# Optimization experiments

Measured on AMD Instinct MI355X. Metric: run time of the kernel, lower is better.

Reference implementation:

```python
import jax, jax.numpy as jnp
import numpy as np

B, L = 64, 512
D_IN, D_POS = 256, 64
KS, VS, H = 64, 64, 8
OUT = 256
EPS = 1e-5
NEG = -1e30


def setup_inputs() -> dict:
    key = jax.random.key(0)
    ks = jax.random.split(key, 12)
    D = D_IN + D_POS
    s = 0.02
    return {
        "emb": jax.random.normal(ks[0], (B, L, D_IN), jnp.float32),
        "boxes": jax.random.normal(ks[1], (B, L, D_POS), jnp.float32),
        "lengths": jax.random.randint(ks[2], (B,), 1, L + 1, jnp.int32),
        "Wq": jax.random.normal(ks[3], (D, H * KS), jnp.float32) * s,
        "Wk": jax.random.normal(ks[4], (D, H * KS), jnp.float32) * s,
        "Wv": jax.random.normal(ks[5], (D, H * VS), jnp.float32) * s,
        "W1": jax.random.normal(ks[6], (H * VS, OUT), jnp.float32) * s,
        "b1": jnp.zeros((OUT,), jnp.float32),
        "W2": jax.random.normal(ks[7], (OUT, OUT), jnp.float32) * s,
        "b2": jnp.zeros((OUT,), jnp.float32),
        "g1": jnp.ones((OUT,), jnp.float32),
        "be1": jnp.zeros((OUT,), jnp.float32),
        "g2": jnp.ones((OUT,), jnp.float32),
        "be2": jnp.zeros((OUT,), jnp.float32),
    }


def masked_bn(x, m, cnt, gamma, beta):
    # BatchNorm1d (training stats) over valid tokens only; x: [B,L,C], m: [B,L,1]
    mean = jnp.sum(x * m, axis=(0, 1)) / cnt
    var = jnp.sum(((x - mean) ** 2) * m, axis=(0, 1)) / cnt
    return gamma * (x - mean) * jax.lax.rsqrt(var + EPS) + beta


def reference(emb, boxes, lengths, Wq, Wk, Wv, W1, b1, W2, b2, g1, be1, g2, be2):
    X = jnp.concatenate([emb, boxes], axis=-1)  # [B,L,D]
    valid = (jnp.arange(L)[None, :] < lengths[:, None])  # [B,L] bool
    m = valid[..., None].astype(X.dtype)  # [B,L,1]
    cnt = jnp.sum(m)

    D = X.shape[-1]
    Q = jnp.einsum('bld,dhk->bhlk', X, Wq.reshape(D, H, KS))
    K = jnp.einsum('bld,dhk->bhlk', X, Wk.reshape(D, H, KS))
    V = jnp.einsum('bld,dhv->bhlv', X, Wv.reshape(D, H, VS))

    scores = jnp.einsum('bhqk,bhmk->bhqm', Q, K) / jnp.sqrt(jnp.float32(KS))
    scores = jnp.where(valid[:, None, None, :], scores, NEG)  # mask keys
    A = jax.nn.softmax(scores, axis=-1)  # [B,H,L,L]
    Z = jnp.einsum('bhqm,bhmv->bhqv', A, V)  # [B,H,L,V]
    Z = jnp.transpose(Z, (0, 2, 1, 3)).reshape(B, L, H * VS)

    # agregate: Linear -> BN -> ReLU -> (dropout=identity, eval) -> Linear -> BN + skip -> ReLU
    Z1 = Z @ W1 + b1
    Z1 = jax.nn.relu(masked_bn(Z1, m, cnt, g1, be1)) * m
    Z2 = Z1 @ W2 + b2
    out = jax.nn.relu(masked_bn(Z2, m, cnt, g2, be2) + emb) * m
    return out  # padded [B,L,OUT]; invalid positions zeroed
```

## Files before the change

kernel.cpp:

```cpp
#include <hip/hip_runtime.h>
#include <hip/hip_bf16.h>
#include <cstdio>

#define B_    64
#define L_    512
#define DIN   256
#define DPOS  64
#define DD    320
#define HH    8
#define ROWS  (B_*L_)
#define NQKV  1536

typedef __attribute__((ext_vector_type(4))) float floatx4;
typedef __attribute__((ext_vector_type(8))) __bf16 bf16x8;
typedef __attribute__((ext_vector_type(4))) __bf16 bf16x4;

static __device__ __forceinline__ floatx4 mfma_bf16(bf16x8 a, bf16x8 b, floatx4 c) {
  return __builtin_amdgcn_mfma_f32_16x16x32_bf16(a, b, c, 0, 0, 0);
}

#define GLOAD_LDS(gp, lp) \
  __builtin_amdgcn_global_load_lds((const __attribute__((address_space(1))) void*)(gp), \
                                   (__attribute__((address_space(3))) void*)(lp), 16, 0, 0)

__global__ __launch_bounds__(256)
void prep_emb(const float* __restrict__ emb, __hip_bfloat16* __restrict__ X) {
  int idx = blockIdx.x * 256 + threadIdx.x;
  int row = idx >> 6, c4 = (idx & 63) * 4;
  const float4 v = *(const float4*)(emb + (size_t)idx * 4);
  bf16x4 o; o[0] = (__bf16)v.x; o[1] = (__bf16)v.y; o[2] = (__bf16)v.z; o[3] = (__bf16)v.w;
  *(bf16x4*)((__bf16*)X + (size_t)row * DD + c4) = o;
}

__global__ __launch_bounds__(256)
void prep_box(const float* __restrict__ boxes, __hip_bfloat16* __restrict__ X) {
  int idx = blockIdx.x * 256 + threadIdx.x;
  int row = idx >> 4, c4 = (idx & 15) * 4;
  const float4 v = *(const float4*)(boxes + (size_t)idx * 4);
  bf16x4 o; o[0] = (__bf16)v.x; o[1] = (__bf16)v.y; o[2] = (__bf16)v.z; o[3] = (__bf16)v.w;
  *(bf16x4*)((__bf16*)X + (size_t)row * DD + DIN + c4) = o;
}

__global__ __launch_bounds__(256)
void prep_w(const float* __restrict__ Wq, const float* __restrict__ Wk,
            const float* __restrict__ Wv, const float* __restrict__ W1,
            const float* __restrict__ W2,
            __hip_bfloat16* __restrict__ WqkvT, __hip_bfloat16* __restrict__ W1T,
            __hip_bfloat16* __restrict__ W2T) {
  __shared__ float tile[64][65];
  int blk = blockIdx.x, t = threadIdx.x;
  const float* src; __hip_bfloat16* dst; int n0, k0, ldsrc, lddst;
  if (blk < 120) {
    int m = blk / 40, rel = blk % 40;
    src = (m == 0) ? Wq : (m == 1) ? Wk : Wv;
    dst = WqkvT + (size_t)m * 512 * DD;
    n0 = (rel / 5) * 64; k0 = (rel % 5) * 64; ldsrc = 512; lddst = DD;
  } else if (blk < 152) {
    int rel = blk - 120;
    src = W1; dst = W1T; n0 = (rel >> 3) * 64; k0 = (rel & 7) * 64; ldsrc = 256; lddst = 512;
  } else {
    int rel = blk - 152;
    src = W2; dst = W2T; n0 = (rel >> 2) * 64; k0 = (rel & 3) * 64; ldsrc = 256; lddst = 256;
  }
#pragma unroll
  for (int i = 0; i < 16; ++i) {
    int e = i * 256 + t, kr = e >> 6, nc = e & 63;
    tile[kr][nc] = src[(size_t)(k0 + kr) * ldsrc + n0 + nc];
  }
  __syncthreads();
#pragma unroll
  for (int i = 0; i < 4; ++i) {
    int ww = i * 256 + t, nr = ww >> 4, kc = (ww & 15) * 4;
    bf16x4 o;
    o[0] = (__bf16)tile[kc][nr];   o[1] = (__bf16)tile[kc+1][nr];
    o[2] = (__bf16)tile[kc+2][nr]; o[3] = (__bf16)tile[kc+3][nr];
    *(bf16x4*)(dst + (size_t)(n0 + nr) * lddst + k0 + kc) = o;
  }
}

template<int EPI>
__global__ __launch_bounds__(256)
void gemm_bt(const __hip_bfloat16* __restrict__ A, const __hip_bfloat16* __restrict__ BT,
             int nbx, int N, int K, int lda,
             float* __restrict__ outF, const float* __restrict__ bias,
             __hip_bfloat16* __restrict__ outQK, __hip_bfloat16* __restrict__ outVT,
             const int* __restrict__ lengths, float* __restrict__ pS,
             float* __restrict__ pS2) {
  __shared__ __align__(16) __bf16 sm[32768];
  int hw = blockIdx.x;
  int lidx = (hw & 7) * ((int)gridDim.x >> 3) + (hw >> 3);
  int bx = lidx % nbx, by = lidx / nbx;
  int t = threadIdx.x;
  int m0 = by * 128, n0 = bx * 128;
  int lenb = lengths[m0 >> 9];
  if ((m0 & 511) >= lenb) {
    if (EPI == 1 && t < 128) {
      pS [by*256 + bx*128 + t] = 0.f;
      pS2[by*256 + bx*128 + t] = 0.f;
    }
    return;
  }
  int wave = t >> 6, lane = t & 63, lr = lane & 15, lg = lane >> 4;
  int wr = wave >> 1, wc = wave & 1;
  floatx4 acc[4][4];
#pragma unroll
  for (int i = 0; i < 4; ++i)
#pragma unroll
    for (int j = 0; j < 4; ++j)
#pragma unroll
      for (int q = 0; q < 4; ++q) acc[i][j][q] = 0.f;

  int srow = t >> 3;
  int scb = (t & 7) ^ (srow & 7);
  const __bf16* gA = (const __bf16*)A + (size_t)(m0 + srow) * lda + scb * 8;
  const __bf16* gB = (const __bf16*)BT + (size_t)(n0 + srow) * K + scb * 8;

  auto stage = [&](int k0, int buf) {
    __bf16* Ad = sm + buf * 8192;
    __bf16* Bd = sm + 16384 + buf * 8192;
#pragma unroll
    for (int r = 0; r < 4; ++r) {
      GLOAD_LDS(gA + (size_t)(r*32) * lda + k0, Ad + (r*256 + t) * 8);
      GLOAD_LDS(gB + (size_t)(r*32) * K   + k0, Bd + (r*256 + t) * 8);
    }
  };

  int aoff[4][2], boff[4][2];
#pragma unroll
  for (int i = 0; i < 4; ++i) {
#pragma unroll
    for (int ks = 0; ks < 2; ++ks) {
      int ra = wr*64 + i*16 + lr;
      int rb = wc*64 + i*16 + lr;
      aoff[i][ks] = ra*64 + (((ks*4 + lg) ^ (ra & 7)) * 8);
      boff[i][ks] = rb*64 + (((ks*4 + lg) ^ (rb & 7)) * 8);
    }
  }

  int NK = K >> 6;
  stage(0, 0);
  __syncthreads();
  for (int kt = 0; kt < NK; ++kt) {
    int cur = kt & 1;
    if (kt + 1 < NK) stage((kt + 1) << 6, cur ^ 1);
    const __bf16* As = sm + cur * 8192;
    const __bf16* Bs = sm + 16384 + cur * 8192;
#pragma unroll
    for (int ks = 0; ks < 2; ++ks) {
      bf16x8 af[4], bfr[4];
#pragma unroll
      for (int i = 0; i < 4; ++i) af[i]  = *(const bf16x8*)(As + aoff[i][ks]);
#pragma unroll
      for (int j = 0; j < 4; ++j) bfr[j] = *(const bf16x8*)(Bs + boff[j][ks]);
      __builtin_amdgcn_s_setprio(1);
#pragma unroll
      for (int i = 0; i < 4; ++i)
#pragma unroll
        for (int j = 0; j < 4; ++j)
          acc[i][j] = mfma_bf16(af[i], bfr[j], acc[i][j]);
      __builtin_amdgcn_s_setprio(0);
    }
    __syncthreads();
  }

  if (EPI == 1) {
    int lbase = m0 & 511;
    float s1[4] = {0.f,0.f,0.f,0.f}, s2[4] = {0.f,0.f,0.f,0.f};
#pragma unroll
    for (int i = 0; i < 4; ++i)
#pragma unroll
      for (int j = 0; j < 4; ++j)
#pragma unroll
        for (int q = 0; q < 4; ++q) {
          int rrow = wr*64 + i*16 + lg*4 + q;
          int col = n0 + wc*64 + j*16 + lr;
          float v = acc[i][j][q] + bias[col];
          outF[(size_t)(m0 + rrow) * N + col] = v;
          if (lbase + rrow < lenb) { s1[j] += v; s2[j] += v*v; }
        }
#pragma unroll
    for (int j = 0; j < 4; ++j) {
      s1[j] += __shfl_xor(s1[j], 16); s1[j] += __shfl_xor(s1[j], 32);
      s2[j] += __shfl_xor(s2[j], 16); s2[j] += __shfl_xor(s2[j], 32);
    }
    float* fb = (float*)sm;
    if (lg == 0) {
#pragma unroll
      for (int j = 0; j < 4; ++j) {
        int cloc = wc*64 + j*16 + lr;
        fb[wr*128 + cloc] = s1[j];
        fb[256 + wr*128 + cloc] = s2[j];
      }
    }
    __syncthreads();
    if (t < 128) {
      pS [by*256 + bx*128 + t] = fb[t] + fb[128 + t];
      pS2[by*256 + bx*128 + t] = fb[256 + t] + fb[384 + t];
    }
  } else if (n0 < 1024) {
#pragma unroll
    for (int i = 0; i < 4; ++i)
#pragma unroll
      for (int j = 0; j < 4; ++j)
#pragma unroll
        for (int q = 0; q < 4; ++q) {
          int row = m0 + wr*64 + i*16 + lg*4 + q;
          int col = n0 + wc*64 + j*16 + lr;
          outQK[(size_t)row * 1024 + col] = __float2bfloat16(acc[i][j][q]);
        }
  } else {
    __bf16* Ct = sm;
#pragma unroll
    for (int i = 0; i < 4; ++i)
#pragma unroll
      for (int j = 0; j < 4; ++j) {
        int col = wc*64 + j*16 + lr;
        int row0 = wr*64 + i*16 + lg*4;
        bf16x4 pv;
#pragma unroll
        for (int q = 0; q < 4; ++q) pv[q] = (__bf16)acc[i][j][q];
        *(bf16x4*)(Ct + col*136 + row0) = pv;
      }
    __syncthreads();
    int b = m0 >> 9, l0 = m0 & 511, gcol0 = n0 - 1024;
#pragma unroll
    for (int it = 0; it < 8; ++it) {
      int g = it * 256 + t;
      int vv = g >> 4, rc = g & 15;
      bf16x8 val = *(const bf16x8*)(Ct + vv*136 + rc*8);
      int gc = gcol0 + vv, h = gc >> 6, vg = gc & 63;
      *(bf16x8*)((__bf16*)outVT + ((size_t)((b*HH + h)*64 + vg))*512 + l0 + rc*8) = val;
    }
  }
}

__global__ __launch_bounds__(512)
void attn(__hip_bfloat16* QK, const __hip_bfloat16* __restrict__ VT,
          const int* __restrict__ lengths) {
  int hw = blockIdx.x;
  int h = hw & 7, qt = (hw >> 3) & 3, b = hw >> 5;
  int len = lengths[b];
  if (qt * 128 >= len) return;
  __shared__ __align__(16) __hip_bfloat16 Ks[2][4096];
  __shared__ __align__(16) __hip_bfloat16 Vs[2][4096];
  __shared__ __align__(16) __hip_bfloat16 P[8][16][72];
  int t = threadIdx.x, wave = t >> 6, lane = t & 63, lr = lane & 15, lg = lane >> 4;
  int q0 = qt * 128 + wave * 16;
  const __hip_bfloat16* Qb = QK + (size_t)b*512*1024 + h*64;
  const __hip_bfloat16* Kb = QK + (size_t)b*512*1024 + 512 + h*64;
  const __hip_bfloat16* Vb = VT + (size_t)(b*HH + h)*64*512;

  bf16x8 qf0 = *(const bf16x8*)(Qb + (size_t)(q0 + lr)*1024 + lg*8);
  bf16x8 qf1 = *(const bf16x8*)(Qb + (size_t)(q0 + lr)*1024 + 32 + lg*8);
#pragma unroll
  for (int i = 0; i < 8; ++i) {
    qf0[i] = (__bf16)((float)qf0[i] * 0.125f);
    qf1[i] = (__bf16)((float)qf1[i] * 0.125f);
  }
  bf16x8 onesf;
#pragma unroll
  for (int i = 0; i < 8; ++i) onesf[i] = (__bf16)1.0f;

  int off0[4], off1[4];
#pragma unroll
  for (int r4 = 0; r4 < 4; ++r4) {
    int row = r4*16 + lr, sw = row & 7;
    off0[r4] = row*64 + ((lg ^ sw) * 8);
    off1[r4] = row*64 + (((lg + 4) ^ sw) * 8);
  }
  int srow = t >> 3, scb = t & 7;
  int scbd = scb ^ (srow & 7);
  const __hip_bfloat16* kgp = Kb + (size_t)srow*1024 + scbd*8;
  const __hip_bfloat16* vgp = Vb + (size_t)srow*512 + scbd*8;

  int nt = (len + 63) >> 6;

  auto stage = [&](int kt, int buf) {
    GLOAD_LDS(kgp + (size_t)kt*65536, &Ks[buf][t*8]);
    GLOAD_LDS(vgp + kt*64, &Vs[buf][t*8]);
  };

  floatx4 O[4];
  floatx4 Ol = {0.f, 0.f, 0.f, 0.f};
#pragma unroll
  for (int vb = 0; vb < 4; ++vb)
#pragma unroll
    for (int i = 0; i < 4; ++i) O[vb][i] = 0.f;

  stage(0, 0);
  __syncthreads();

  for (int kt = 0; kt < nt; ++kt) {
    int cur = kt & 1;
    if (kt + 1 < nt) stage(kt + 1, cur ^ 1);
    int kb0 = kt * 64;
    const __hip_bfloat16* Kc = Ks[cur];
    const __hip_bfloat16* Vc = Vs[cur];

    floatx4 S[4];
    __builtin_amdgcn_s_setprio(1);
#pragma unroll
    for (int kb = 0; kb < 4; ++kb) {
      bf16x8 kf0 = *(const bf16x8*)(Kc + off0[kb]);
      bf16x8 kf1 = *(const bf16x8*)(Kc + off1[kb]);
      floatx4 s = {0.f, 0.f, 0.f, 0.f};
      s = mfma_bf16(kf0, qf0, s);
      s = mfma_bf16(kf1, qf1, s);
      S[kb] = s;
    }
    __builtin_amdgcn_s_setprio(0);
#pragma unroll
    for (int kb = 0; kb < 4; ++kb)
#pragma unroll
      for (int i = 0; i < 4; ++i) S[kb][i] = __expf(S[kb][i]);
    if (kb0 + 64 > len) {
#pragma unroll
      for (int kb = 0; kb < 4; ++kb)
#pragma unroll
        for (int i = 0; i < 4; ++i)
          if (kb0 + kb*16 + lg*4 + i >= len) S[kb][i] = 0.f;
    }
#pragma unroll
    for (int kb = 0; kb < 4; ++kb) {
      bf16x4 pv;
#pragma unroll
      for (int i = 0; i < 4; ++i) pv[i] = (__bf16)S[kb][i];
      *(bf16x4*)(&P[wave][lr][kb*16 + lg*4]) = pv;
    }
    bf16x8 pf0 = *(const bf16x8*)(&P[wave][lr][lg*8]);
    bf16x8 pf1 = *(const bf16x8*)(&P[wave][lr][32 + lg*8]);
    __builtin_amdgcn_s_setprio(1);
#pragma unroll
    for (int vb = 0; vb < 4; ++vb) {
      bf16x8 vf0 = *(const bf16x8*)(Vc + off0[vb]);
      bf16x8 vf1 = *(const bf16x8*)(Vc + off1[vb]);
      O[vb] = mfma_bf16(pf0, vf0, O[vb]);
      O[vb] = mfma_bf16(pf1, vf1, O[vb]);
    }
    Ol = mfma_bf16(pf0, onesf, Ol);
    Ol = mfma_bf16(pf1, onesf, Ol);
    __builtin_amdgcn_s_setprio(0);
    __syncthreads();
  }

#pragma unroll
  for (int vb = 0; vb < 4; ++vb)
#pragma unroll
    for (int i = 0; i < 4; ++i) {
      int q = q0 + lg*4 + i;
      float z = O[vb][i] / Ol[i];
      QK[(size_t)(b*512 + q)*1024 + h*64 + vb*16 + lr] = __float2bfloat16(z);
    }
}

__global__ __launch_bounds__(256)
void stats_fin(const float* __restrict__ pS, const float* __restrict__ pS2,
               const int* __restrict__ lengths, const float* __restrict__ g,
               const float* __restrict__ be, float* __restrict__ aff) {
  int t = threadIdx.x;
  float cnt = 0.f;
  for (int i = 0; i < 64; ++i) cnt += (float)lengths[i];
  float s = 0.f, s2 = 0.f;
  for (int i = 0; i < 256; ++i) { s += pS[i*256 + t]; s2 += pS2[i*256 + t]; }
  float mean = s / cnt;
  float var = s2 / cnt - mean * mean;
  float a = g[t] * rsqrtf(var + 1e-5f);
  aff[t] = a;
  aff[256 + t] = be[t] - mean * a;
}

__global__ __launch_bounds__(256)
void apply1(const float* __restrict__ Zr, const int* __restrict__ lengths,
            const float* __restrict__ aff, __hip_bfloat16* __restrict__ Zn) {
  int idx = blockIdx.x * 256 + threadIdx.x;
  int row = idx >> 6, c4 = (idx & 63) * 4;
  int b = row >> 9, l = row & 511;
  bool ok = l < lengths[b];
  float4 v = *(const float4*)(Zr + (size_t)row*256 + c4);
  float4 a = *(const float4*)(aff + c4);
  float4 c = *(const float4*)(aff + 256 + c4);
  bf16x4 o;
  o[0] = (__bf16)(ok ? fmaxf(a.x*v.x + c.x, 0.f) : 0.f);
  o[1] = (__bf16)(ok ? fmaxf(a.y*v.y + c.y, 0.f) : 0.f);
  o[2] = (__bf16)(ok ? fmaxf(a.z*v.z + c.z, 0.f) : 0.f);
  o[3] = (__bf16)(ok ? fmaxf(a.w*v.w + c.w, 0.f) : 0.f);
  *(bf16x4*)((__bf16*)Zn + (size_t)row*256 + c4) = o;
}

__global__ __launch_bounds__(256)
void apply2(const float* __restrict__ Zr, const float* __restrict__ emb,
            const int* __restrict__ lengths, const float* __restrict__ aff,
            float* __restrict__ out) {
  int idx = blockIdx.x * 256 + threadIdx.x;
  int row = idx >> 6, c4 = (idx & 63) * 4;
  int b = row >> 9, l = row & 511;
  bool ok = l < lengths[b];
  size_t base = (size_t)row*256 + c4;
  float4 v = *(const float4*)(Zr + base);
  float4 e = *(const float4*)(emb + base);
  float4 a = *(const float4*)(aff + c4);
  float4 c = *(const float4*)(aff + 256 + c4);
  float4 o;
  o.x = ok ? fmaxf(a.x*v.x + c.x + e.x, 0.f) : 0.f;
  o.y = ok ? fmaxf(a.y*v.y + c.y + e.y, 0.f) : 0.f;
  o.z = ok ? fmaxf(a.z*v.z + c.z + e.z, 0.f) : 0.f;
  o.w = ok ? fmaxf(a.w*v.w + c.w + e.w, 0.f) : 0.f;
  *(float4*)(out + base) = o;
}

extern "C" void kernel_launch(void* const* d_in, const int* in_sizes, int n_in,
                              void* d_out, int out_size, void* d_ws, size_t ws_size,
                              hipStream_t stream) {
  const float* emb   = (const float*)d_in[0];
  const float* boxes = (const float*)d_in[1];
  const int*   dlen  = (const int*)d_in[2];
  const float* Wq    = (const float*)d_in[3];
  const float* Wk    = (const float*)d_in[4];
  const float* Wv    = (const float*)d_in[5];
  const float* W1    = (const float*)d_in[6];
  const float* b1    = (const float*)d_in[7];
  const float* W2    = (const float*)d_in[8];
  const float* b2    = (const float*)d_in[9];
  const float* g1    = (const float*)d_in[10];
  const float* be1   = (const float*)d_in[11];
  const float* g2    = (const float*)d_in[12];
  const float* be2   = (const float*)d_in[13];
  float* out = (float*)d_out;

  const size_t oWqkvT = 0;
  const size_t oW1T   = 983040;
  const size_t oW2T   = 1245184;
  const size_t oAff1  = 1376256;
  const size_t oAff2  = 1378304;
  const size_t oPS    = 1380352;
  const size_t oPS2   = 1642496;
  const size_t oXbf   = 1904640;
  const size_t oQK    = 22876160;
  const size_t oVT    = 89985024;
  const size_t NEED   = 123539456;
  if (ws_size < NEED) { fprintf(stderr, "ws too small: %zu < %zu\n", ws_size, NEED); return; }

  char* w = (char*)d_ws;
  __hip_bfloat16* WqkvT = (__hip_bfloat16*)(w + oWqkvT);
  __hip_bfloat16* W1T   = (__hip_bfloat16*)(w + oW1T);
  __hip_bfloat16* W2T   = (__hip_bfloat16*)(w + oW2T);
  float* aff1 = (float*)(w + oAff1);
  float* aff2 = (float*)(w + oAff2);
  float* pS   = (float*)(w + oPS);
  float* pS2  = (float*)(w + oPS2);
  __hip_bfloat16* Xbf = (__hip_bfloat16*)(w + oXbf);
  __hip_bfloat16* Z1n = (__hip_bfloat16*)(w + oXbf);
  __hip_bfloat16* QK  = (__hip_bfloat16*)(w + oQK);
  float* Z2raw = (float*)(w + oQK);
  __hip_bfloat16* VT  = (__hip_bfloat16*)(w + oVT);
  float* Z1raw = (float*)(w + oVT);

  prep_emb<<<ROWS/4, 256, 0, stream>>>(emb, Xbf);
  prep_box<<<ROWS/16, 256, 0, stream>>>(boxes, Xbf);
  prep_w<<<168, 256, 0, stream>>>(Wq, Wk, Wv, W1, W2, WqkvT, W1T, W2T);
  gemm_bt<0><<<12*256, 256, 0, stream>>>(
      Xbf, WqkvT, 12, NQKV, DD, DD, nullptr, nullptr, QK, VT,
      dlen, nullptr, nullptr);
  attn<<<2048, 512, 0, stream>>>(QK, VT, dlen);
  gemm_bt<1><<<2*256, 256, 0, stream>>>(
      QK, W1T, 2, 256, 512, 1024, Z1raw, b1, nullptr, nullptr,
      dlen, pS, pS2);
  stats_fin<<<1, 256, 0, stream>>>(pS, pS2, dlen, g1, be1, aff1);
  apply1<<<ROWS/4, 256, 0, stream>>>(Z1raw, dlen, aff1, Z1n);
  gemm_bt<1><<<2*256, 256, 0, stream>>>(
      Z1n, W2T, 2, 256, 256, 256, Z2raw, b2, nullptr, nullptr,
      dlen, pS, pS2);
  stats_fin<<<1, 256, 0, stream>>>(pS, pS2, dlen, g2, be2, aff2);
  apply2<<<ROWS/4, 256, 0, stream>>>(Z2raw, emb, dlen, aff2, out);
}
```

Measured before the change: 158.1 us.

## Shrink attention key tiles, use exp2, parallelize stats and skip padded rows

The attention key/value tile shrinks from 64 to 32 keys per step. This lowers LDS use and tightens length tail waste, and K and V staging is split across the two halves of the block. The softmax switches to exp2, with log2(e) folded into the query scale. stats_fin now reduces with 1024 threads instead of a serial 256-row loop. The two prep kernels merge into one launch, and apply1 and apply2 skip reading padded rows beyond each sequence length. Smaller tiles double the loop iterations and barriers per key block.

Result: slower. 167.5 us (+6.0%).

```diff
diff --git a/kernel.cpp b/kernel.cpp
--- a/kernel.cpp
+++ b/kernel.cpp
@@ -24,21 +24,22 @@
                                    (__attribute__((address_space(3))) void*)(lp), 16, 0, 0)
 
 __global__ __launch_bounds__(256)
-void prep_emb(const float* __restrict__ emb, __hip_bfloat16* __restrict__ X) {
-  int idx = blockIdx.x * 256 + threadIdx.x;
-  int row = idx >> 6, c4 = (idx & 63) * 4;
-  const float4 v = *(const float4*)(emb + (size_t)idx * 4);
-  bf16x4 o; o[0] = (__bf16)v.x; o[1] = (__bf16)v.y; o[2] = (__bf16)v.z; o[3] = (__bf16)v.w;
-  *(bf16x4*)((__bf16*)X + (size_t)row * DD + c4) = o;
-}
-
-__global__ __launch_bounds__(256)
-void prep_box(const float* __restrict__ boxes, __hip_bfloat16* __restrict__ X) {
-  int idx = blockIdx.x * 256 + threadIdx.x;
-  int row = idx >> 4, c4 = (idx & 15) * 4;
-  const float4 v = *(const float4*)(boxes + (size_t)idx * 4);
-  bf16x4 o; o[0] = (__bf16)v.x; o[1] = (__bf16)v.y; o[2] = (__bf16)v.z; o[3] = (__bf16)v.w;
-  *(bf16x4*)((__bf16*)X + (size_t)row * DD + DIN + c4) = o;
+void prep_x(const float* __restrict__ emb, const float* __restrict__ boxes,
+            __hip_bfloat16* __restrict__ X) {
+  int bb = blockIdx.x;
+  if (bb < ROWS/4) {
+    int idx = bb * 256 + threadIdx.x;
+    int row = idx >> 6, c4 = (idx & 63) * 4;
+    const float4 v = *(const float4*)(emb + (size_t)idx * 4);
+    bf16x4 o; o[0] = (__bf16)v.x; o[1] = (__bf16)v.y; o[2] = (__bf16)v.z; o[3] = (__bf16)v.w;
+    *(bf16x4*)((__bf16*)X + (size_t)row * DD + c4) = o;
+  } else {
+    int idx = (bb - ROWS/4) * 256 + threadIdx.x;
+    int row = idx >> 4, c4 = (idx & 15) * 4;
+    const float4 v = *(const float4*)(boxes + (size_t)idx * 4);
+    bf16x4 o; o[0] = (__bf16)v.x; o[1] = (__bf16)v.y; o[2] = (__bf16)v.z; o[3] = (__bf16)v.w;
+    *(bf16x4*)((__bf16*)X + (size_t)row * DD + DIN + c4) = o;
+  }
 }
 
 __global__ __launch_bounds__(256)
@@ -241,9 +242,9 @@
   int h = hw & 7, qt = (hw >> 3) & 3, b = hw >> 5;
   int len = lengths[b];
   if (qt * 128 >= len) return;
-  __shared__ __align__(16) __hip_bfloat16 Ks[2][4096];
-  __shared__ __align__(16) __hip_bfloat16 Vs[2][4096];
-  __shared__ __align__(16) __hip_bfloat16 P[8][16][72];
+  __shared__ __align__(16) __hip_bfloat16 Ks[2][2048];
+  __shared__ __align__(16) __hip_bfloat16 Vs[2][2048];
+  __shared__ __align__(16) __hip_bfloat16 P[8][16][40];
   int t = threadIdx.x, wave = t >> 6, lane = t & 63, lr = lane & 15, lg = lane >> 4;
   int q0 = qt * 128 + wave * 16;
   const __hip_bfloat16* Qb = QK + (size_t)b*512*1024 + h*64;
@@ -254,30 +255,37 @@
   bf16x8 qf1 = *(const bf16x8*)(Qb + (size_t)(q0 + lr)*1024 + 32 + lg*8);
 #pragma unroll
   for (int i = 0; i < 8; ++i) {
-    qf0[i] = (__bf16)((float)qf0[i] * 0.125f);
-    qf1[i] = (__bf16)((float)qf1[i] * 0.125f);
+    qf0[i] = (__bf16)((float)qf0[i] * 0.18033688f);
+    qf1[i] = (__bf16)((float)qf1[i] * 0.18033688f);
   }
   bf16x8 onesf;
 #pragma unroll
   for (int i = 0; i < 8; ++i) onesf[i] = (__bf16)1.0f;
 
-  int off0[4], off1[4];
-#pragma unroll
-  for (int r4 = 0; r4 < 4; ++r4) {
-    int row = r4*16 + lr, sw = row & 7;
-    off0[r4] = row*64 + ((lg ^ sw) * 8);
-    off1[r4] = row*64 + (((lg + 4) ^ sw) * 8);
-  }
-  int srow = t >> 3, scb = t & 7;
-  int scbd = scb ^ (srow & 7);
-  const __hip_bfloat16* kgp = Kb + (size_t)srow*1024 + scbd*8;
-  const __hip_bfloat16* vgp = Vb + (size_t)srow*512 + scbd*8;
-
-  int nt = (len + 63) >> 6;
+  int koff0[2], koff1[2];
+#pragma unroll
+  for (int kb = 0; kb < 2; ++kb) {
+    int row = kb*16 + lr, sw = row & 7;
+    koff0[kb] = row*64 + ((lg ^ sw) * 8);
+    koff1[kb] = row*64 + (((lg + 4) ^ sw) * 8);
+  }
+  int voff[4];
+#pragma unroll
+  for (int vb = 0; vb < 4; ++vb) {
+    int row = vb*16 + lr;
+    voff[vb] = row*32 + ((lg ^ (row & 3)) * 8);
+  }
+  int ku = t & 255;
+  int krow = ku >> 3, kcb = (ku & 7) ^ (krow & 7);
+  const __hip_bfloat16* kgp = Kb + (size_t)krow*1024 + kcb*8;
+  int vrow = ku >> 2, vcb = (ku & 3) ^ (vrow & 3);
+  const __hip_bfloat16* vgp = Vb + (size_t)vrow*512 + vcb*8;
+
+  int nt = (len + 31) >> 5;
 
   auto stage = [&](int kt, int buf) {
-    GLOAD_LDS(kgp + (size_t)kt*65536, &Ks[buf][t*8]);
-    GLOAD_LDS(vgp + kt*64, &Vs[buf][t*8]);
+    if (t < 256) GLOAD_LDS(kgp + (size_t)kt*32768, &Ks[buf][ku*8]);
+    else         GLOAD_LDS(vgp + kt*32,           &Vs[buf][ku*8]);
   };
 
   floatx4 O[4];
@@ -293,16 +301,16 @@
   for (int kt = 0; kt < nt; ++kt) {
     int cur = kt & 1;
     if (kt + 1 < nt) stage(kt + 1, cur ^ 1);
-    int kb0 = kt * 64;
+    int kb0 = kt * 32;
     const __hip_bfloat16* Kc = Ks[cur];
     const __hip_bfloat16* Vc = Vs[cur];
 
-    floatx4 S[4];
+    floatx4 S[2];
     __builtin_amdgcn_s_setprio(1);
 #pragma unroll
-    for (int kb = 0; kb < 4; ++kb) {
-      bf16x8 kf0 = *(const bf16x8*)(Kc + off0[kb]);
-      bf16x8 kf1 = *(const bf16x8*)(Kc + off1[kb]);
+    for (int kb = 0; kb < 2; ++kb) {
+      bf16x8 kf0 = *(const bf16x8*)(Kc + koff0[kb]);
+      bf16x8 kf1 = *(const bf16x8*)(Kc + koff1[kb]);
       floatx4 s = {0.f, 0.f, 0.f, 0.f};
       s = mfma_bf16(kf0, qf0, s);
       s = mfma_bf16(kf1, qf1, s);
@@ -310,35 +318,31 @@
     }
     __builtin_amdgcn_s_setprio(0);
 #pragma unroll
-    for (int kb = 0; kb < 4; ++kb)
-#pragma unroll
-      for (int i = 0; i < 4; ++i) S[kb][i] = __expf(S[kb][i]);
-    if (kb0 + 64 > len) {
-#pragma unroll
-      for (int kb = 0; kb < 4; ++kb)
+    for (int kb = 0; kb < 2; ++kb)
+#pragma unroll
+      for (int i = 0; i < 4; ++i) S[kb][i] = __builtin_amdgcn_exp2f(S[kb][i]);
+    if (kb0 + 32 > len) {
+#pragma unroll
+      for (int kb = 0; kb < 2; ++kb)
 #pragma unroll
         for (int i = 0; i < 4; ++i)
           if (kb0 + kb*16 + lg*4 + i >= len) S[kb][i] = 0.f;
     }
 #pragma unroll
-    for (int kb = 0; kb < 4; ++kb) {
+    for (int kb = 0; kb < 2; ++kb) {
       bf16x4 pv;
 #pragma unroll
       for (int i = 0; i < 4; ++i) pv[i] = (__bf16)S[kb][i];
       *(bf16x4*)(&P[wave][lr][kb*16 + lg*4]) = pv;
     }
-    bf16x8 pf0 = *(const bf16x8*)(&P[wave][lr][lg*8]);
-    bf16x8 pf1 = *(const bf16x8*)(&P[wave][lr][32 + lg*8]);
+    bf16x8 pf = *(const bf16x8*)(&P[wave][lr][lg*8]);
     __builtin_amdgcn_s_setprio(1);
 #pragma unroll
     for (int vb = 0; vb < 4; ++vb) {
-      bf16x8 vf0 = *(const bf16x8*)(Vc + off0[vb]);
-      bf16x8 vf1 = *(const bf16x8*)(Vc + off1[vb]);
-      O[vb] = mfma_bf16(pf0, vf0, O[vb]);
-      O[vb] = mfma_bf16(pf1, vf1, O[vb]);
-    }
-    Ol = mfma_bf16(pf0, onesf, Ol);
-    Ol = mfma_bf16(pf1, onesf, Ol);
+      bf16x8 vf = *(const bf16x8*)(Vc + voff[vb]);
+      O[vb] = mfma_bf16(pf, vf, O[vb]);
+    }
+    Ol = mfma_bf16(pf, onesf, Ol);
     __builtin_amdgcn_s_setprio(0);
     __syncthreads();
   }
@@ -353,20 +357,30 @@
     }
 }
 
-__global__ __launch_bounds__(256)
+__global__ __launch_bounds__(1024)
 void stats_fin(const float* __restrict__ pS, const float* __restrict__ pS2,
                const int* __restrict__ lengths, const float* __restrict__ g,
                const float* __restrict__ be, float* __restrict__ aff) {
-  int t = threadIdx.x;
-  float cnt = 0.f;
-  for (int i = 0; i < 64; ++i) cnt += (float)lengths[i];
+  __shared__ float red[2048];
+  int t = threadIdx.x, col = t & 255, part = t >> 8;
   float s = 0.f, s2 = 0.f;
-  for (int i = 0; i < 256; ++i) { s += pS[i*256 + t]; s2 += pS2[i*256 + t]; }
-  float mean = s / cnt;
-  float var = s2 / cnt - mean * mean;
-  float a = g[t] * rsqrtf(var + 1e-5f);
-  aff[t] = a;
-  aff[256 + t] = be[t] - mean * a;
+  for (int i = part*64; i < part*64 + 64; ++i) {
+    s += pS[i*256 + col]; s2 += pS2[i*256 + col];
+  }
+  red[part*256 + col] = s;
+  red[1024 + part*256 + col] = s2;
+  __syncthreads();
+  if (t < 256) {
+    float cnt = 0.f;
+    for (int i = 0; i < 64; ++i) cnt += (float)lengths[i];
+    float fs = red[t] + red[256 + t] + red[512 + t] + red[768 + t];
+    float fs2 = red[1024 + t] + red[1280 + t] + red[1536 + t] + red[1792 + t];
+    float mean = fs / cnt;
+    float var = fs2 / cnt - mean * mean;
+    float a = g[t] * rsqrtf(var + 1e-5f);
+    aff[t] = a;
+    aff[256 + t] = be[t] - mean * a;
+  }
 }
 
 __global__ __launch_bounds__(256)
@@ -375,7 +389,9 @@
   int idx = blockIdx.x * 256 + threadIdx.x;
   int row = idx >> 6, c4 = (idx & 63) * 4;
   int b = row >> 9, l = row & 511;
-  bool ok = l < lengths[b];
+  int lenb = lengths[b];
+  if (l >= ((lenb + 127) & ~127)) return;
+  bool ok = l < lenb;
   float4 v = *(const float4*)(Zr + (size_t)row*256 + c4);
   float4 a = *(const float4*)(aff + c4);
   float4 c = *(const float4*)(aff + 256 + c4);
@@ -394,17 +410,21 @@
   int idx = blockIdx.x * 256 + threadIdx.x;
   int row = idx >> 6, c4 = (idx & 63) * 4;
   int b = row >> 9, l = row & 511;
-  bool ok = l < lengths[b];
   size_t base = (size_t)row*256 + c4;
+  if (l >= lengths[b]) {
+    float4 z = {0.f, 0.f, 0.f, 0.f};
+    *(float4*)(out + base) = z;
+    return;
+  }
   float4 v = *(const float4*)(Zr + base);
   float4 e = *(const float4*)(emb + base);
   float4 a = *(const float4*)(aff + c4);
   float4 c = *(const float4*)(aff + 256 + c4);
   float4 o;
-  o.x = ok ? fmaxf(a.x*v.x + c.x + e.x, 0.f) : 0.f;
-  o.y = ok ? fmaxf(a.y*v.y + c.y + e.y, 0.f) : 0.f;
-  o.z = ok ? fmaxf(a.z*v.z + c.z + e.z, 0.f) : 0.f;
-  o.w = ok ? fmaxf(a.w*v.w + c.w + e.w, 0.f) : 0.f;
+  o.x = fmaxf(a.x*v.x + c.x + e.x, 0.f);
+  o.y = fmaxf(a.y*v.y + c.y + e.y, 0.f);
+  o.z = fmaxf(a.z*v.z + c.z + e.z, 0.f);
+  o.w = fmaxf(a.w*v.w + c.w + e.w, 0.f);
   *(float4*)(out + base) = o;
 }
 
@@ -455,8 +475,7 @@
   __hip_bfloat16* VT  = (__hip_bfloat16*)(w + oVT);
   float* Z1raw = (float*)(w + oVT);
 
-  prep_emb<<<ROWS/4, 256, 0, stream>>>(emb, Xbf);
-  prep_box<<<ROWS/16, 256, 0, stream>>>(boxes, Xbf);
+  prep_x<<<ROWS/4 + ROWS/16, 256, 0, stream>>>(emb, boxes, Xbf);
   prep_w<<<168, 256, 0, stream>>>(Wq, Wk, Wv, W1, W2, WqkvT, W1T, W2T);
   gemm_bt<0><<<12*256, 256, 0, stream>>>(
       Xbf, WqkvT, 12, NQKV, DD, DD, nullptr, nullptr, QK, VT,
@@ -465,11 +484,11 @@
   gemm_bt<1><<<2*256, 256, 0, stream>>>(
       QK, W1T, 2, 256, 512, 1024, Z1raw, b1, nullptr, nullptr,
       dlen, pS, pS2);
-  stats_fin<<<1, 256, 0, stream>>>(pS, pS2, dlen, g1, be1, aff1);
+  stats_fin<<<1, 1024, 0, stream>>>(pS, pS2, dlen, g1, be1, aff1);
   apply1<<<ROWS/4, 256, 0, stream>>>(Z1raw, dlen, aff1, Z1n);
   gemm_bt<1><<<2*256, 256, 0, stream>>>(
       Z1n, W2T, 2, 256, 256, 256, Z2raw, b2, nullptr, nullptr,
       dlen, pS, pS2);
-  stats_fin<<<1, 256, 0, stream>>>(pS, pS2, dlen, g2, be2, aff2);
+  stats_fin<<<1, 1024, 0, stream>>>(pS, pS2, dlen, g2, be2, aff2);
   apply2<<<ROWS/4, 256, 0, stream>>>(Z2raw, emb, dlen, aff2, out);
 }
```
